# Performance work log

Measured on AMD Instinct MI355X. Metric: run time of the kernel, lower is better.

## Reference

```python
import jax, jax.numpy as jnp
import numpy as np

# Layer widths parsed from arch "1024-4096-4096-32000"
LENS = [1024, 4096, 4096, 32000]
SIZES = [1048576, 1048576, 4194304]
# Per-layer hash constants (odd primes); chosen so i*A + j*B + C stays < 2^31 (int32 safe)
HASH_A = [9973, 10007, 10039]
HASH_B = [31013, 31019, 31039]
HASH_C = [557, 563, 569]


def _virtual_weight(hw, in_dim, out_dim, a, b, c):
    """Reconstruct the [in_dim, out_dim] virtual weight by modular hashing
    into the flat compressed vector hw (ROBE-Z, chunk size 1)."""
    i = jnp.arange(in_dim, dtype=jnp.int32)[:, None]
    j = jnp.arange(out_dim, dtype=jnp.int32)[None, :]
    idx = (i * a + j * b + c) % hw.shape[0]  # irregular gather indices
    return hw[idx]  # [in_dim, out_dim]


def setup_inputs() -> dict:
    key = jax.random.key(0)
    kx, k0, k1, k2 = jax.random.split(key, 4)
    x = jax.random.normal(kx, (2048, LENS[0]), dtype=jnp.float32)
    hws = {}
    for l, kk in enumerate([k0, k1, k2]):
        bound = 1.0 / np.sqrt(LENS[l + 1])
        hws[f"hw{l}"] = jax.random.uniform(
            kk, (SIZES[l],), dtype=jnp.float32, minval=-bound, maxval=bound)
    return {"x": x, **hws}


def reference(x, hw0, hw1, hw2):
    hws = [hw0, hw1, hw2]
    h = x
    for l in range(3):
        W = _virtual_weight(hws[l], LENS[l], LENS[l + 1],
                            HASH_A[l], HASH_B[l], HASH_C[l])
        h = h @ W  # [B, out_dim]
        if l < 2:  # ReLU between layers only (self.layers[:-1] drops final ReLU)
            h = jax.nn.relu(h)
    return h
```

## Files before the change

kernel.cpp:

```cpp
#include <hip/hip_runtime.h>
#include <stdint.h>

typedef __attribute__((ext_vector_type(8))) short bf16x8;
typedef __attribute__((ext_vector_type(4))) float f32x4;

__device__ __forceinline__ ushort f2bf(float f) {
  union { float f; uint32_t u; } v; v.f = f;
  return (ushort)((v.u + 0x7FFFu + ((v.u >> 16) & 1u)) >> 16);
}

__device__ __forceinline__ void load_lds16(const void* g, void* l) {
  __builtin_amdgcn_global_load_lds(
      (const __attribute__((address_space(1))) void*)g,
      (__attribute__((address_space(3))) void*)l, 16, 0, 0);
}

template <int N>
__device__ __forceinline__ void waitvm() {
  asm volatile("s_waitcnt vmcnt(%0)" :: "n"(N) : "memory");
}

__global__ void cvt_bf16_kernel(const float4* __restrict__ x, ushort4* __restrict__ o, int n4) {
  int i = blockIdx.x * blockDim.x + threadIdx.x;
  int stride = gridDim.x * blockDim.x;
  for (; i < n4; i += stride) {
    float4 v = x[i];
    o[i] = make_ushort4(f2bf(v.x), f2bf(v.y), f2bf(v.z), f2bf(v.w));
  }
}

template <int A, int B, int CC, int M, int K, int SL>
__global__ __launch_bounds__(512) void mat_lds_kernel(
    const float* __restrict__ t, ushort* __restrict__ wt, int n0, int nc, int bps) {
  const int sub = blockIdx.x / bps;
  const int blk = blockIdx.x - sub * bps;
  const int lo = sub * SL;
  __shared__ float sl[SL];
  {
    const float* src = t + lo;
    const int tid = threadIdx.x;
#pragma unroll
    for (int it4 = 0; it4 < SL / 4; it4 += 512) {
      load_lds16(src + (size_t)(it4 + tid) * 4, (char*)sl + (size_t)(it4 + tid) * 16);
    }
  }
  asm volatile("s_waitcnt vmcnt(0)" ::: "memory");
  __syncthreads();

  const int w = threadIdx.x >> 6, lane = threadIdx.x & 63;
  const int jq = lane >> 2, pos = lane & 3;
  constexpr int J = (int)(((long)(K - 1) * A + (M - 1)) / M) + 1;
  constexpr int BIAS = 1024;
  const int rpb = (nc + bps - 1) / bps;
  const int rlo = blk * rpb;
  const int rhi = (nc < rlo + rpb) ? nc : (rlo + rpb);

#pragma unroll 2
  for (int r = rlo + w; r < rhi; r += 8) {
    const int n = n0 + r;
    const int offs = (int)(((unsigned)((long)n * B + CC)) & (unsigned)(M - 1));
    ushort* wrow = wt + (size_t)r * K;
#pragma unroll
    for (int jb = 0; jb < J; jb += 16) {
      const int jj = jb + jq;
      const int D = jj * M + lo - offs;
      const int kL = (int)((unsigned)(D + A * BIAS + A - 1) / (unsigned)A) - BIAS;
      const int kU = (int)((unsigned)(D + SL + A * BIAS + A - 1) / (unsigned)A) - BIAS;
      const int k = kL + pos;
      if (k < kU && k < K && k >= 0) {
        const int idx = k * A - D;
        wrow[k] = f2bf(sl[idx]);
      }
    }
  }
}

__device__ __forceinline__ void stq(const ushort* src, size_t qstep, int q,
                                    ushort* dstbase, int tid) {
  load_lds16(src + (size_t)q * qstep, dstbase + q * 4096 + tid * 8);
}

template <int BM, bool F32OUT>
__global__ __launch_bounds__(512, 2) void gemm256(
    const ushort* __restrict__ Ag, const ushort* __restrict__ Bg,
    float* __restrict__ Cf, ushort* __restrict__ Ch,
    int K, int ldc, int colbase, int mtiles) {
  constexpr int NA = BM / 64;
  constexpr int MS = BM / 128;
  constexpr int MR = BM / 32;
  constexpr int AE = BM * 64;
  constexpr int BE = 256 * 64;
  constexpr int BUF = AE + BE;
  __shared__ alignas(16) ushort lds[2 * BUF];
  const int tid = threadIdx.x;
  const int lane = tid & 63, w = tid >> 6;
  const int wr = w >> 2, wc = w & 3;
  const int fr = lane & 15, fq = lane >> 4, l7 = lane & 7;

  const int nwg = (int)gridDim.x, bid = (int)blockIdx.x;
  const int q8 = nwg >> 3, r8 = nwg & 7;
  const int xcd = bid & 7, ix = bid >> 3;
  const int swz = (xcd < r8 ? xcd * (q8 + 1) : r8 * (q8 + 1) + (xcd - r8) * q8) + ix;
  const int m0 = (swz % mtiles) * BM;
  const int n0 = (swz / mtiles) * 256;

  const int rowq = tid >> 3;
  const int cswz = ((tid & 7) ^ (rowq & 7)) * 8;
  const ushort* sA = Ag + (size_t)(m0 + rowq) * K + cswz;
  const ushort* sB = Bg + (size_t)(n0 + rowq) * K + cswz;
  const size_t qstep = (size_t)64 * (size_t)K;

  const int au0 = ((0 * 4 + fq) ^ l7) * 8;
  const int au1 = ((1 * 4 + fq) ^ l7) * 8;
  const int abase = (wr * 16 + fr) * 64;
  const int bbase = (wc * 64 + fr) * 64;

  f32x4 acc[MR][4] = {};
  bf16x8 aF[2][2], bF[4][2];

  {
    ushort* nAv = lds;
    ushort* nBv = lds + AE;
    stq(sB, qstep, 0, nBv, tid); stq(sB, qstep, 1, nBv, tid);
    stq(sB, qstep, 2, nBv, tid); stq(sB, qstep, 3, nBv, tid);
#pragma unroll
    for (int q = 0; q < NA; ++q) stq(sA, qstep, q, nAv, tid);
    sA += 64; sB += 64;
  }
  waitvm<NA - 1>();
  __builtin_amdgcn_s_barrier();
  {
    const ushort* pB = lds + AE;
#pragma unroll
    for (int nj = 0; nj < 4; ++nj) {
      bF[nj][0] = *(const bf16x8*)(pB + bbase + nj * 1024 + au0);
      bF[nj][1] = *(const bf16x8*)(pB + bbase + nj * 1024 + au1);
    }
  }

#define RDSUB(P)                                                        \
  _Pragma("unroll")                                                     \
  for (int mi2 = 0; mi2 < MS; ++mi2) {                                  \
    aF[mi2][0] = *(const bf16x8*)(bAv + abase + ((P) * MS + mi2) * 2048 + au0); \
    aF[mi2][1] = *(const bf16x8*)(bAv + abase + ((P) * MS + mi2) * 2048 + au1); \
  }

#define MFMAPH(P)                                                       \
  __builtin_amdgcn_s_setprio(1);                                        \
  _Pragma("unroll")                                                     \
  for (int kk = 0; kk < 2; ++kk) {                                      \
    _Pragma("unroll")                                                   \
    for (int mi2 = 0; mi2 < MS; ++mi2) {                                \
      _Pragma("unroll")                                                 \
      for (int nj = 0; nj < 4; ++nj)                                    \
        acc[(P) * MS + mi2][nj] = __builtin_amdgcn_mfma_f32_16x16x32_bf16( \
            aF[mi2][kk], bF[nj][kk], acc[(P) * MS + mi2][nj], 0, 0, 0); \
    }                                                                   \
  }                                                                     \
  __builtin_amdgcn_s_setprio(0);

  const int T = K >> 6;
#pragma unroll 1
  for (int t = 0; t < T; ++t) {
    const int b = t & 1;
    ushort* bAv = lds + b * BUF;
    ushort* nAv = lds + (b ^ 1) * BUF;
    ushort* nBv = nAv + AE;
    const bool pre = (t + 1 < T);

    RDSUB(0);
    if (pre) { stq(sB, qstep, 0, nBv, tid); stq(sB, qstep, 1, nBv, tid);
               if (BM == 256) waitvm<4>(); }
    else     { if (BM == 256) waitvm<2>(); }
    __builtin_amdgcn_s_barrier();
    MFMAPH(0);
    __builtin_amdgcn_s_barrier();

    RDSUB(1);
    if (pre) { stq(sB, qstep, 2, nBv, tid); stq(sB, qstep, 3, nBv, tid);
               waitvm<(BM == 256) ? 5 : 4>(); }
    else     { waitvm<(BM == 256) ? 1 : 0>(); }
    __builtin_amdgcn_s_barrier();
    MFMAPH(1);
    __builtin_amdgcn_s_barrier();

    RDSUB(2);
    if (pre) {
#pragma unroll
      for (int q = 0; q < NA / 2; ++q) stq(sA, qstep, q, nAv, tid);
      if (BM == 256) waitvm<6>();
    } else { if (BM == 256) waitvm<0>(); }
    __builtin_amdgcn_s_barrier();
    MFMAPH(2);
    __builtin_amdgcn_s_barrier();

    RDSUB(3);
    if (pre) {
#pragma unroll
      for (int q = NA / 2; q < NA; ++q) stq(sA, qstep, q, nAv, tid);
      waitvm<(BM == 256) ? 3 : 1>();
    }
    __builtin_amdgcn_s_barrier();
    MFMAPH(3);
    if (pre) {
#pragma unroll
      for (int nj = 0; nj < 4; ++nj) {
        bF[nj][0] = *(const bf16x8*)(nBv + bbase + nj * 1024 + au0);
        bF[nj][1] = *(const bf16x8*)(nBv + bbase + nj * 1024 + au1);
      }
    }
    __builtin_amdgcn_s_barrier();

    if (pre) { sA += 64; sB += 64; }
  }
#undef RDSUB
#undef MFMAPH

#pragma unroll
  for (int mi = 0; mi < MR; ++mi)
#pragma unroll
    for (int nj = 0; nj < 4; ++nj)
#pragma unroll
      for (int e = 0; e < 4; ++e) {
        int row = m0 + wr * 16 + mi * 32 + fq * 4 + e;
        int col = colbase + n0 + wc * 64 + nj * 16 + fr;
        float v = acc[mi][nj][e];
        if (F32OUT) {
          Cf[(size_t)row * ldc + col] = v;
        } else {
          v = v > 0.0f ? v : 0.0f;
          Ch[(size_t)row * ldc + col] = f2bf(v);
        }
      }
}

template <int A, int B, int CC, int M, int K, int BM, bool F32OUT>
static void run_layer256(const ushort* Ain, const float* tbl, ushort* hOut, float* fOut,
                         int N, int ldc, ushort* wb, size_t avail, hipStream_t stream) {
  constexpr int SL = 1 << 15;
  constexpr int NSUB = M / SL;
  const int bps = (NSUB >= 256) ? 1 : (256 / NSUB);
  long ncmax = (long)(avail / (size_t)((size_t)K * 2));
  ncmax = (ncmax / 256) * 256;
  if (ncmax > N) ncmax = N;
  if (ncmax < 256) ncmax = 256;
  const int mtiles = 2048 / BM;
  for (int n0 = 0; n0 < N; n0 += (int)ncmax) {
    int nc = (N - n0 < (int)ncmax) ? (N - n0) : (int)ncmax;
    hipLaunchKernelGGL((mat_lds_kernel<A, B, CC, M, K, SL>),
                       dim3((unsigned)(NSUB * bps)), dim3(512), 0, stream,
                       tbl, wb, n0, nc, bps);
    dim3 g((unsigned)((nc / 256) * mtiles));
    hipLaunchKernelGGL((gemm256<BM, F32OUT>), g, dim3(512), 0, stream,
                       Ain, wb, fOut, hOut, K, ldc, n0, mtiles);
  }
}

extern "C" void kernel_launch(void* const* d_in, const int* in_sizes, int n_in,
                              void* d_out, int out_size, void* d_ws, size_t ws_size,
                              hipStream_t stream) {
  const float* x   = (const float*)d_in[0];
  const float* hw0 = (const float*)d_in[1];
  const float* hw1 = (const float*)d_in[2];
  const float* hw2 = (const float*)d_in[3];
  float* out = (float*)d_out;
  uint8_t* ws = (uint8_t*)d_ws;

  ushort* xb = (ushort*)(ws + 0);
  ushort* h1 = (ushort*)(ws + ((size_t)4 << 20));
  ushort* h2 = (ushort*)(ws + ((size_t)20 << 20));
  ushort* wb = (ushort*)(ws + ((size_t)36 << 20));
  size_t avail = ws_size > ((size_t)36 << 20) ? ws_size - ((size_t)36 << 20)
                                              : (size_t)(128 * 4096 * 2);

  hipLaunchKernelGGL(cvt_bf16_kernel, dim3(1024), dim3(256), 0, stream,
                     (const float4*)x, (ushort4*)xb, 2048 * 1024 / 4);

  run_layer256<9973, 31013, 557, 1 << 20, 1024, 128, false>(
      xb, hw0, h1, nullptr, 4096, 4096, wb, avail, stream);
  run_layer256<10007, 31019, 563, 1 << 20, 4096, 128, false>(
      h1, hw1, h2, nullptr, 4096, 4096, wb, avail, stream);
  run_layer256<10039, 31039, 569, 1 << 22, 4096, 256, true>(
      h2, hw2, nullptr, out, 32000, 32000, wb, avail, stream);
}
```

Baseline: 897.4 us.

## Add software-pipelined 256x256 GEMM for the final layer with XCD-aware tile swizzle

```diff
diff --git a/kernel.cpp b/kernel.cpp
--- a/kernel.cpp
+++ b/kernel.cpp
@@ -234,7 +234,129 @@
       }
 }
 
-template <int A, int B, int CC, int M, int K, int BM, bool F32OUT>
+__global__ __launch_bounds__(512, 2) void gemm256p(
+    const ushort* __restrict__ Ag, const ushort* __restrict__ Bg,
+    float* __restrict__ Cf, int K, int ldc, int colbase, int mtiles) {
+  __shared__ alignas(16) ushort lds[2 * 32768];
+  const int tid = threadIdx.x;
+  const int lane = tid & 63, w = tid >> 6;
+  const int wr = w >> 2, wc = w & 3;
+  const int fr = lane & 15, fq = lane >> 4, l7 = lane & 7;
+
+  const int nwg = (int)gridDim.x, bid = (int)blockIdx.x;
+  const int q8 = nwg >> 3, r8 = nwg & 7;
+  const int xcd = bid & 7, ix = bid >> 3;
+  const int swz = (xcd < r8 ? xcd * (q8 + 1) : r8 * (q8 + 1) + (xcd - r8) * q8) + ix;
+  const int m0 = (swz % mtiles) * 256;
+  const int n0 = (swz / mtiles) * 256;
+
+  const int rowq = tid >> 3;
+  const int cswz = ((tid & 7) ^ (rowq & 7)) * 8;
+  const ushort* sA = Ag + (size_t)(m0 + rowq) * K + cswz;
+  const int rB1 = ((rowq >> 5) << 6) + (rowq & 31);
+  const ushort* sB = Bg + (size_t)(n0 + rB1) * K + cswz;
+  const size_t qstep = (size_t)64 * (size_t)K;
+  const size_t Ksz = (size_t)K;
+
+  const int au0 = ((0 * 4 + fq) ^ l7) * 8;
+  const int au1 = ((1 * 4 + fq) ^ l7) * 8;
+  const int abase = (wr * 16 + fr) * 64;
+  const int bbase2 = (wc * 32 + fr) * 64;
+
+  f32x4 acc[8][4] = {};
+  bf16x8 aH[4][2], bH0[2][2], bH1[2][2];
+
+#define STA(bufb, h, g, kt)                                             \
+  load_lds16(sA + (size_t)((h) * 2 + (g)) * qstep + (size_t)(kt) * 64,  \
+             (char*)&lds[(bufb) * 32768 + (h) * 8192 + (g) * 4096 + tid * 8]);
+#define STB(bufb, h, g, kt)                                             \
+  load_lds16(sB + (size_t)((g) * 128 + (h) * 32) * Ksz + (size_t)(kt) * 64, \
+             (char*)&lds[(bufb) * 32768 + 16384 + (h) * 8192 + (g) * 4096 + tid * 8]);
+#define RDA(bufb, miH)                                                  \
+  _Pragma("unroll")                                                     \
+  for (int mi2 = 0; mi2 < 4; ++mi2) {                                   \
+    aH[mi2][0] = *(const bf16x8*)&lds[(bufb) * 32768 + ((miH) * 4 + mi2) * 2048 + abase + au0]; \
+    aH[mi2][1] = *(const bf16x8*)&lds[(bufb) * 32768 + ((miH) * 4 + mi2) * 2048 + abase + au1]; \
+  }
+#define RDB(bufb, njH, dst)                                             \
+  _Pragma("unroll")                                                     \
+  for (int j1 = 0; j1 < 2; ++j1) {                                      \
+    dst[j1][0] = *(const bf16x8*)&lds[(bufb) * 32768 + 16384 + (njH) * 8192 + bbase2 + j1 * 1024 + au0]; \
+    dst[j1][1] = *(const bf16x8*)&lds[(bufb) * 32768 + 16384 + (njH) * 8192 + bbase2 + j1 * 1024 + au1]; \
+  }
+#define MF(miH, njH, bArr)                                              \
+  __builtin_amdgcn_s_setprio(1);                                        \
+  _Pragma("unroll")                                                     \
+  for (int kk = 0; kk < 2; ++kk) {                                      \
+    _Pragma("unroll")                                                   \
+    for (int mi2 = 0; mi2 < 4; ++mi2) {                                 \
+      _Pragma("unroll")                                                 \
+      for (int j1 = 0; j1 < 2; ++j1)                                    \
+        acc[(miH) * 4 + mi2][(njH) * 2 + j1] = __builtin_amdgcn_mfma_f32_16x16x32_bf16( \
+            aH[mi2][kk], bArr[j1][kk], acc[(miH) * 4 + mi2][(njH) * 2 + j1], 0, 0, 0); \
+    }                                                                   \
+  }                                                                     \
+  __builtin_amdgcn_s_setprio(0);
+
+  STA(0, 0, 0, 0); STA(0, 0, 1, 0);
+  STB(0, 0, 0, 0); STB(0, 0, 1, 0);
+  STA(0, 1, 0, 0); STA(0, 1, 1, 0);
+  STB(0, 1, 0, 0); STB(0, 1, 1, 0);
+  STA(1, 0, 0, 1); STA(1, 0, 1, 1);
+  STB(1, 0, 0, 1); STB(1, 0, 1, 1);
+  waitvm<8>();
+  __builtin_amdgcn_s_barrier();
+
+  const int T = K >> 6;
+#pragma unroll 1
+  for (int t = 0; t < T; ++t) {
+    const int b = t & 1, nb = b ^ 1;
+    const bool p1 = (t + 1 < T), p2 = (t + 2 < T);
+
+    RDA(b, 0); RDB(b, 0, bH0);
+    if (p1) { STA(nb, 1, 0, t + 1); STA(nb, 1, 1, t + 1); waitvm<6>(); }
+    else    { waitvm<0>(); }
+    __builtin_amdgcn_s_barrier();
+    MF(0, 0, bH0);
+    __builtin_amdgcn_s_barrier();
+
+    RDB(b, 1, bH1);
+    if (p1) { STB(nb, 1, 0, t + 1); STB(nb, 1, 1, t + 1); }
+    __builtin_amdgcn_s_barrier();
+    MF(0, 1, bH1);
+    __builtin_amdgcn_s_barrier();
+
+    RDA(b, 1);
+    if (p2) { STA(b, 0, 0, t + 2); STA(b, 0, 1, t + 2); }
+    __builtin_amdgcn_s_barrier();
+    MF(1, 0, bH0);
+    __builtin_amdgcn_s_barrier();
+
+    if (p2)      { STB(b, 0, 0, t + 2); STB(b, 0, 1, t + 2); waitvm<8>(); }
+    else if (p1) { waitvm<4>(); }
+    __builtin_amdgcn_s_barrier();
+    MF(1, 1, bH1);
+    __builtin_amdgcn_s_barrier();
+  }
+#undef STA
+#undef STB
+#undef RDA
+#undef RDB
+#undef MF
+
+#pragma unroll
+  for (int mi = 0; mi < 8; ++mi)
+#pragma unroll
+    for (int nj = 0; nj < 4; ++nj)
+#pragma unroll
+      for (int e = 0; e < 4; ++e) {
+        int row = m0 + wr * 16 + mi * 32 + fq * 4 + e;
+        int col = colbase + n0 + wc * 64 + nj * 16 + fr;
+        Cf[(size_t)row * ldc + col] = acc[mi][nj][e];
+      }
+}
+
+template <int A, int B, int CC, int M, int K, int BM, bool F32OUT, bool PIPE>
 static void run_layer256(const ushort* Ain, const float* tbl, ushort* hOut, float* fOut,
                          int N, int ldc, ushort* wb, size_t avail, hipStream_t stream) {
   constexpr int SL = 1 << 15;
@@ -251,8 +373,12 @@
                        dim3((unsigned)(NSUB * bps)), dim3(512), 0, stream,
                        tbl, wb, n0, nc, bps);
     dim3 g((unsigned)((nc / 256) * mtiles));
-    hipLaunchKernelGGL((gemm256<BM, F32OUT>), g, dim3(512), 0, stream,
-                       Ain, wb, fOut, hOut, K, ldc, n0, mtiles);
+    if (PIPE)
+      hipLaunchKernelGGL(gemm256p, g, dim3(512), 0, stream,
+                         Ain, wb, fOut, K, ldc, n0, mtiles);
+    else
+      hipLaunchKernelGGL((gemm256<BM, F32OUT>), g, dim3(512), 0, stream,
+                         Ain, wb, fOut, hOut, K, ldc, n0, mtiles);
   }
 }
 
@@ -276,10 +402,10 @@
   hipLaunchKernelGGL(cvt_bf16_kernel, dim3(1024), dim3(256), 0, stream,
                      (const float4*)x, (ushort4*)xb, 2048 * 1024 / 4);
 
-  run_layer256<9973, 31013, 557, 1 << 20, 1024, 128, false>(
+  run_layer256<9973, 31013, 557, 1 << 20, 1024, 128, false, false>(
       xb, hw0, h1, nullptr, 4096, 4096, wb, avail, stream);
-  run_layer256<10007, 31019, 563, 1 << 20, 4096, 128, false>(
+  run_layer256<10007, 31019, 563, 1 << 20, 4096, 128, false, false>(
       h1, hw1, h2, nullptr, 4096, 4096, wb, avail, stream);
-  run_layer256<10039, 31039, 569, 1 << 22, 4096, 256, true>(
+  run_layer256<10039, 31039, 569, 1 << 22, 4096, 256, true, true>(
       h2, hw2, nullptr, out, 32000, 32000, wb, avail, stream);
 }
```

Result: no change. 889.7 us (median of 3 runs) (-0.9%).
